# Kernel tuning notes

Measured on AMD Instinct MI355X. Metric: run time of the kernel, lower is better.

## Reference

```python
import jax, jax.numpy as jnp
import numpy as np

POSE_DIM, H_DIM, LATENT_DIM, NUM_LAYERS = 96, 32, 16, 2
BATCH, OBS_LEN, PRED_LEN = 16384, 16, 25


def setup_inputs() -> dict:
    key = jax.random.key(0)
    ks = jax.random.split(key, 16)
    s = 0.1
    inp = {
        "obs_s": jax.random.normal(ks[0], (OBS_LEN, BATCH, POSE_DIM), jnp.float32),
        "latent": jax.random.normal(ks[1], (BATCH, LATENT_DIM), jnp.float32),
        "pred_len": PRED_LEN,
        # FC: latent_dim -> h_dim
        "W_fc": jax.random.normal(ks[2], (H_DIM, LATENT_DIM), jnp.float32) * s,
        "b_fc": jnp.zeros((H_DIM,), jnp.float32),
        # LSTM layer 0 (input pose_dim), PyTorch gate order i,f,g,o
        "W_ih0": jax.random.normal(ks[3], (4 * H_DIM, POSE_DIM), jnp.float32) * s,
        "W_hh0": jax.random.normal(ks[4], (4 * H_DIM, H_DIM), jnp.float32) * s,
        "b_ih0": jax.random.normal(ks[5], (4 * H_DIM,), jnp.float32) * s,
        "b_hh0": jax.random.normal(ks[6], (4 * H_DIM,), jnp.float32) * s,
        # LSTM layer 1 (input h_dim)
        "W_ih1": jax.random.normal(ks[7], (4 * H_DIM, H_DIM), jnp.float32) * s,
        "W_hh1": jax.random.normal(ks[8], (4 * H_DIM, H_DIM), jnp.float32) * s,
        "b_ih1": jax.random.normal(ks[9], (4 * H_DIM,), jnp.float32) * s,
        "b_hh1": jax.random.normal(ks[10], (4 * H_DIM,), jnp.float32) * s,
        # mlp: h_dim -> pose_dim
        "W_mlp": jax.random.normal(ks[11], (POSE_DIM, H_DIM), jnp.float32) * s,
        "b_mlp": jnp.zeros((POSE_DIM,), jnp.float32),
    }
    return inp


def _lstm_cell(x, h, c, W_ih, W_hh, b):
    # x: [B, in], h/c: [B, H]; gates in PyTorch order i, f, g, o
    gates = x @ W_ih.T + h @ W_hh.T + b
    i, f, g, o = jnp.split(gates, 4, axis=-1)
    c_new = jax.nn.sigmoid(f) * c + jax.nn.sigmoid(i) * jnp.tanh(g)
    h_new = jax.nn.sigmoid(o) * jnp.tanh(c_new)
    return h_new, c_new


def reference(obs_s, latent, pred_len, W_fc, b_fc,
              W_ih0, W_hh0, b_ih0, b_hh0,
              W_ih1, W_hh1, b_ih1, b_hh1,
              W_mlp, b_mlp):
    batch = obs_s.shape[1]
    h_init = latent @ W_fc.T + b_fc                    # [B, H] -> both layers
    c0 = jnp.zeros((batch, H_DIM), obs_s.dtype)
    b0 = b_ih0 + b_hh0
    b1 = b_ih1 + b_hh1

    def step(carry, _):
        last, h0, c0_, h1, c1_ = carry
        h0, c0_ = _lstm_cell(last, h0, c0_, W_ih0, W_hh0, b0)
        h1, c1_ = _lstm_cell(h0, h1, c1_, W_ih1, W_hh1, b1)
        curr = h1 @ W_mlp.T + b_mlp                    # [B, pose_dim]
        return (curr, h0, c0_, h1, c1_), curr

    init = (obs_s[-1], h_init, c0, h_init, c0)
    _, preds = jax.lax.scan(step, init, None, length=pred_len)
    return preds  # [pred_len, B, pose_dim]
```

## Files before the change

### kernel.cpp

```cpp
#include <hip/hip_runtime.h>


#define PRED 25
#define BATCH 16384
#define ET    16
#define XROW  192
#define HROW  128
#define LROW  64

typedef unsigned short u16;
typedef unsigned int   u32;
typedef __attribute__((ext_vector_type(8))) short bf16x8;
typedef __attribute__((ext_vector_type(4))) float f32x4;

__device__ __forceinline__ float fast_rcp(float x){ return __builtin_amdgcn_rcpf(x); }
__device__ __forceinline__ float sigm(float x){ return fast_rcp(1.0f + __expf(-x)); }
__device__ __forceinline__ float tanh_(float x){ return 1.0f - 2.0f*fast_rcp(__expf(2.0f*x) + 1.0f); }
__device__ __forceinline__ u16 f2b(float f){
  u32 i = __float_as_uint(f);
  i += 0x7FFFu + ((i >> 16) & 1u);
  return (u16)(i >> 16);
}
__device__ __forceinline__ float b2f(u16 u){ return __uint_as_float(((u32)u) << 16); }

struct __align__(16) SM {
  u16 xh[ET*XROW];
  u16 hh[ET*HROW];
  u16 h1lo[ET*LROW];
};

__device__ __forceinline__ int swx(int e, int k){ return e*XROW + (k ^ ((e&7)<<3)); }
__device__ __forceinline__ int swh(int e, int k){ return e*HROW + (k ^ ((e&7)<<3)); }
__device__ __forceinline__ int swl(int e, int k){ return e*LROW + (k ^ ((e&7)<<3)); }

__device__ __forceinline__ bf16x8 pack8(float4 f0, float4 f1){
  union { bf16x8 v; u16 u8[8]; } fr;
  fr.u8[0]=f2b(f0.x); fr.u8[1]=f2b(f0.y); fr.u8[2]=f2b(f0.z); fr.u8[3]=f2b(f0.w);
  fr.u8[4]=f2b(f1.x); fr.u8[5]=f2b(f1.y); fr.u8[6]=f2b(f1.z); fr.u8[7]=f2b(f1.w);
  return fr.v;
}

extern "C" __global__ __launch_bounds__(128, 2)
void decoder_kernel(const float* __restrict__ obs,  const float* __restrict__ lat,
                    const float* __restrict__ Wfc,  const float* __restrict__ bfc,
                    const float* __restrict__ Wih0, const float* __restrict__ Whh0,
                    const float* __restrict__ bih0, const float* __restrict__ bhh0,
                    const float* __restrict__ Wih1, const float* __restrict__ Whh1,
                    const float* __restrict__ bih1, const float* __restrict__ bhh1,
                    const float* __restrict__ Wmlp, const float* __restrict__ bmlp,
                    float* __restrict__ out)
{
  __shared__ SM sm;
  const int tid = threadIdx.x;
  const int ebase = blockIdx.x * ET;
  const int mh = tid >> 6;
  const int l  = tid & 63;
  const int lr = l & 15;
  const int kq = l >> 4;
  const int e_ln = lr;

  {
    int e = tid >> 3, c8 = (tid & 7)*12;
    const float* src = obs + ((size_t)(15*BATCH) + ebase + e)*96 + c8;
    float4 a = *(const float4*)(src);
    float4 b = *(const float4*)(src+4);
    float4 c = *(const float4*)(src+8);
    float v[12] = {a.x,a.y,a.z,a.w,b.x,b.y,b.z,b.w,c.x,c.y,c.z,c.w};
    #pragma unroll
    for (int j = 0; j < 6; ++j){
      u32 pk = (u32)f2b(v[2*j]) | ((u32)f2b(v[2*j+1]) << 16);
      *(u32*)&sm.xh[swx(e, c8 + 2*j)] = pk;
    }
  }
  {
    int u = tid & 31, eb = (tid >> 5)*4;
    const float* wf = Wfc + u*16;
    float bb = bfc[u];
    #pragma unroll
    for (int e4 = 0; e4 < 4; ++e4){
      int e = eb + e4;
      const float* lp = lat + (size_t)(ebase + e)*16;
      float a = bb;
      #pragma unroll
      for (int j = 0; j < 16; ++j) a = fmaf(wf[j], lp[j], a);
      u16 hb = f2b(a);
      sm.xh[swx(e, 96 + u)] = hb;
      sm.hh[swh(e, 32 + u)] = hb;
    }
  }

  bf16x8 aw0[4][4];
  #pragma unroll
  for (int i = 0; i < 4; ++i){
    int vg = (mh*4 + i)*16 + lr;
    int g  = (vg & 3)*32 + (vg >> 2);
    #pragma unroll
    for (int c = 0; c < 4; ++c){
      int k = c*32 + kq*8;
      const float* src = (k < 96) ? (Wih0 + g*96 + k) : (Whh0 + g*32 + (k - 96));
      aw0[i][c] = pack8(*(const float4*)src, *(const float4*)(src+4));
    }
  }
  bf16x8 aw1[4][2];
  #pragma unroll
  for (int i = 0; i < 4; ++i){
    int vg = (mh*4 + i)*16 + lr;
    int g  = (vg & 3)*32 + (vg >> 2);
    #pragma unroll
    for (int c = 0; c < 2; ++c){
      int k = c*32 + kq*8;
      const float* src = (k < 32) ? (Wih1 + g*32 + k) : (Whh1 + g*32 + (k - 32));
      aw1[i][c] = pack8(*(const float4*)src, *(const float4*)(src+4));
    }
  }
  bf16x8 awm[3];
  #pragma unroll
  for (int i = 0; i < 3; ++i){
    int o = (mh*3 + i)*16 + lr;
    const float* src = Wmlp + o*32 + kq*8;
    awm[i] = pack8(*(const float4*)src, *(const float4*)(src+4));
  }

  f32x4 bias0v[4], bias1v[4];
  #pragma unroll
  for (int i = 0; i < 4; ++i){
    int u = (mh*4 + i)*4 + kq;
    #pragma unroll
    for (int r = 0; r < 4; ++r){
      int g = r*32 + u;
      bias0v[i][r] = bih0[g] + bhh0[g];
      bias1v[i][r] = bih1[g] + bhh1[g];
    }
  }
  f32x4 biasmv[3];
  #pragma unroll
  for (int i = 0; i < 3; ++i){
    int o0 = (mh*3 + i)*16 + kq*4;
    #pragma unroll
    for (int r = 0; r < 4; ++r) biasmv[i][r] = bmlp[o0 + r];
  }

  float c0s[4] = {0.f,0.f,0.f,0.f};
  float c1s[4] = {0.f,0.f,0.f,0.f};

  __syncthreads();

  f32x4 am[3];
  bool have_out = false;
  float* outb = nullptr;

  for (int t = 0; t < PRED; ++t){
    const int p = t & 1;
    bf16x8 bx0 = *(const bf16x8*)&sm.xh[swx(e_ln, 0*32 + kq*8)];
    bf16x8 bx1 = *(const bf16x8*)&sm.xh[swx(e_ln, 1*32 + kq*8)];
    bf16x8 bx2 = *(const bf16x8*)&sm.xh[swx(e_ln, 2*32 + kq*8)];
    bf16x8 bx3 = *(const bf16x8*)&sm.xh[swx(e_ln, 96 + 32*p + kq*8)];
    f32x4 g0[4];
    #pragma unroll
    for (int i = 0; i < 4; ++i){
      f32x4 a = bias0v[i];
      a = __builtin_amdgcn_mfma_f32_16x16x32_bf16(aw0[i][0], bx0, a, 0, 0, 0);
      a = __builtin_amdgcn_mfma_f32_16x16x32_bf16(aw0[i][1], bx1, a, 0, 0, 0);
      a = __builtin_amdgcn_mfma_f32_16x16x32_bf16(aw0[i][2], bx2, a, 0, 0, 0);
      a = __builtin_amdgcn_mfma_f32_16x16x32_bf16(aw0[i][3], bx3, a, 0, 0, 0);
      g0[i] = a;
    }
    #pragma unroll
    for (int i = 0; i < 4; ++i){
      float ig = sigm(g0[i][0]);
      float fg = sigm(g0[i][1]);
      float gg = tanh_(g0[i][2]);
      float og = sigm(g0[i][3]);
      float cn = fmaf(fg, c0s[i], ig*gg);
      c0s[i] = cn;
      u16 hb = f2b(og * tanh_(cn));
      int u = (mh*4 + i)*4 + kq;
      sm.xh[swx(e_ln, 96 + 32*(p^1) + u)] = hb;
      sm.hh[swh(e_ln, u)] = hb;
    }
    __syncthreads();
    bf16x8 bh0 = *(const bf16x8*)&sm.hh[swh(e_ln, kq*8)];
    bf16x8 bh1 = *(const bf16x8*)&sm.hh[swh(e_ln, 32 + 32*p + kq*8)];
    f32x4 g1[4];
    #pragma unroll
    for (int i = 0; i < 4; ++i){
      f32x4 a = bias1v[i];
      a = __builtin_amdgcn_mfma_f32_16x16x32_bf16(aw1[i][0], bh0, a, 0, 0, 0);
      a = __builtin_amdgcn_mfma_f32_16x16x32_bf16(aw1[i][1], bh1, a, 0, 0, 0);
      g1[i] = a;
    }
    #pragma unroll
    for (int i = 0; i < 4; ++i){
      float ig = sigm(g1[i][0]);
      float fg = sigm(g1[i][1]);
      float gg = tanh_(g1[i][2]);
      float og = sigm(g1[i][3]);
      float cn = fmaf(fg, c1s[i], ig*gg);
      c1s[i] = cn;
      float h1 = og * tanh_(cn);
      u16 hi = f2b(h1);
      u16 lo = f2b(h1 - b2f(hi));
      int u = (mh*4 + i)*4 + kq;
      sm.hh[swh(e_ln, 32 + 32*(p^1) + u)] = hi;
      sm.h1lo[swl(e_ln, u)] = lo;
    }
    __syncthreads();
    bf16x8 bmh = *(const bf16x8*)&sm.hh[swh(e_ln, 32 + 32*(p^1) + kq*8)];
    bf16x8 bml = *(const bf16x8*)&sm.h1lo[swl(e_ln, kq*8)];
    #pragma unroll
    for (int i = 0; i < 3; ++i){
      f32x4 a = biasmv[i];
      a = __builtin_amdgcn_mfma_f32_16x16x32_bf16(awm[i], bmh, a, 0, 0, 0);
      a = __builtin_amdgcn_mfma_f32_16x16x32_bf16(awm[i], bml, a, 0, 0, 0);
      am[i] = a;
      int o0 = (mh*3 + i)*16 + kq*4;
      u32 pk01 = (u32)f2b(a[0]) | ((u32)f2b(a[1]) << 16);
      u32 pk23 = (u32)f2b(a[2]) | ((u32)f2b(a[3]) << 16);
      *(u32*)&sm.xh[swx(e_ln, o0)]     = pk01;
      *(u32*)&sm.xh[swx(e_ln, o0 + 2)] = pk23;
    }
    outb = out + (size_t)t*BATCH*96 + (size_t)(ebase + e_ln)*96;
    have_out = true;
    __syncthreads();
    #pragma unroll
    for (int i = 0; i < 3; ++i){
      int o0 = (mh*3 + i)*16 + kq*4;
      *(f32x4*)(outb + o0) = am[i];
    }
  }
  (void)have_out;
}

extern "C" void kernel_launch(void* const* d_in, const int* in_sizes, int n_in,
                              void* d_out, int out_size, void* d_ws, size_t ws_size,
                              hipStream_t stream){
  decoder_kernel<<<dim3(BATCH/ET), dim3(128), 0, stream>>>(
      (const float*)d_in[0],  (const float*)d_in[1],
      (const float*)d_in[3],  (const float*)d_in[4],
      (const float*)d_in[5],  (const float*)d_in[6],
      (const float*)d_in[7],  (const float*)d_in[8],
      (const float*)d_in[9],  (const float*)d_in[10],
      (const float*)d_in[11], (const float*)d_in[12],
      (const float*)d_in[13], (const float*)d_in[14],
      (float*)d_out);
}
```

Measured before the change: 80.56 us.

## Collapse decoder block to a single wave and fold log2e into gate weights

```diff
diff --git a/kernel.cpp b/kernel.cpp
--- a/kernel.cpp
+++ b/kernel.cpp
@@ -3,19 +3,21 @@
 
 #define PRED 25
 #define BATCH 16384
-#define ET    16
-#define XROW  192
-#define HROW  128
-#define LROW  64
+#define SROW 192
 
 typedef unsigned short u16;
 typedef unsigned int   u32;
 typedef __attribute__((ext_vector_type(8))) short bf16x8;
 typedef __attribute__((ext_vector_type(4))) float f32x4;
 
-__device__ __forceinline__ float fast_rcp(float x){ return __builtin_amdgcn_rcpf(x); }
-__device__ __forceinline__ float sigm(float x){ return fast_rcp(1.0f + __expf(-x)); }
-__device__ __forceinline__ float tanh_(float x){ return 1.0f - 2.0f*fast_rcp(__expf(2.0f*x) + 1.0f); }
+#define LOG2E  1.44269504088896340736f
+#define LOG2E2 2.88539008177792681472f
+
+__device__ __forceinline__ float rcp_(float x){ return __builtin_amdgcn_rcpf(x); }
+__device__ __forceinline__ float ex2(float x){ return __builtin_amdgcn_exp2f(x); }
+__device__ __forceinline__ float sigm2(float xp){ return rcp_(1.0f + ex2(-xp)); }
+__device__ __forceinline__ float tanh2(float xp){ return 1.0f - 2.0f*rcp_(ex2(xp) + 1.0f); }
+
 __device__ __forceinline__ u16 f2b(float f){
   u32 i = __float_as_uint(f);
   i += 0x7FFFu + ((i >> 16) & 1u);
@@ -23,24 +25,18 @@
 }
 __device__ __forceinline__ float b2f(u16 u){ return __uint_as_float(((u32)u) << 16); }
 
-struct __align__(16) SM {
-  u16 xh[ET*XROW];
-  u16 hh[ET*HROW];
-  u16 h1lo[ET*LROW];
-};
-
-__device__ __forceinline__ int swx(int e, int k){ return e*XROW + (k ^ ((e&7)<<3)); }
-__device__ __forceinline__ int swh(int e, int k){ return e*HROW + (k ^ ((e&7)<<3)); }
-__device__ __forceinline__ int swl(int e, int k){ return e*LROW + (k ^ ((e&7)<<3)); }
-
-__device__ __forceinline__ bf16x8 pack8(float4 f0, float4 f1){
-  union { bf16x8 v; u16 u8[8]; } fr;
-  fr.u8[0]=f2b(f0.x); fr.u8[1]=f2b(f0.y); fr.u8[2]=f2b(f0.z); fr.u8[3]=f2b(f0.w);
-  fr.u8[4]=f2b(f1.x); fr.u8[5]=f2b(f1.y); fr.u8[6]=f2b(f1.z); fr.u8[7]=f2b(f1.w);
+__device__ __forceinline__ int swz(int e, int k){ return e*SROW + (k ^ ((e&7)<<3)); }
+
+#define LGKM_FENCE() asm volatile("s_waitcnt lgkmcnt(0)" ::: "memory")
+
+__device__ __forceinline__ bf16x8 pack8s(const float* src, float s){
+  union { bf16x8 v; u16 h[8]; } fr;
+  #pragma unroll
+  for (int j = 0; j < 8; ++j) fr.h[j] = f2b(src[j]*s);
   return fr.v;
 }
 
-extern "C" __global__ __launch_bounds__(128, 2)
+extern "C" __global__ __launch_bounds__(64, 1)
 void decoder_kernel(const float* __restrict__ obs,  const float* __restrict__ lat,
                     const float* __restrict__ Wfc,  const float* __restrict__ bfc,
                     const float* __restrict__ Wih0, const float* __restrict__ Whh0,
@@ -50,191 +46,172 @@
                     const float* __restrict__ Wmlp, const float* __restrict__ bmlp,
                     float* __restrict__ out)
 {
-  __shared__ SM sm;
-  const int tid = threadIdx.x;
-  const int ebase = blockIdx.x * ET;
-  const int mh = tid >> 6;
-  const int l  = tid & 63;
+  __shared__ u16 state[16*SROW];
+  const int l  = threadIdx.x;
+  const int ebase = blockIdx.x * 16;
   const int lr = l & 15;
-  const int kq = l >> 4;
-  const int e_ln = lr;
+  const int rq = l >> 4;
 
   {
-    int e = tid >> 3, c8 = (tid & 7)*12;
-    const float* src = obs + ((size_t)(15*BATCH) + ebase + e)*96 + c8;
-    float4 a = *(const float4*)(src);
-    float4 b = *(const float4*)(src+4);
-    float4 c = *(const float4*)(src+8);
-    float v[12] = {a.x,a.y,a.z,a.w,b.x,b.y,b.z,b.w,c.x,c.y,c.z,c.w};
-    #pragma unroll
-    for (int j = 0; j < 6; ++j){
-      u32 pk = (u32)f2b(v[2*j]) | ((u32)f2b(v[2*j+1]) << 16);
-      *(u32*)&sm.xh[swx(e, c8 + 2*j)] = pk;
+    int e = l >> 2, c = (l & 3) * 24;
+    const float* src = obs + ((size_t)(15*BATCH) + ebase + e)*96 + c;
+    #pragma unroll
+    for (int j = 0; j < 12; ++j){
+      float2 v = *(const float2*)(src + 2*j);
+      u32 pk = (u32)f2b(v.x) | ((u32)f2b(v.y) << 16);
+      *(u32*)&state[swz(e, c + 2*j)] = pk;
     }
   }
   {
-    int u = tid & 31, eb = (tid >> 5)*4;
+    int u = l >> 1, eh = (l & 1)*8;
     const float* wf = Wfc + u*16;
     float bb = bfc[u];
     #pragma unroll
-    for (int e4 = 0; e4 < 4; ++e4){
-      int e = eb + e4;
+    for (int r = 0; r < 8; ++r){
+      int e = eh + r;
       const float* lp = lat + (size_t)(ebase + e)*16;
       float a = bb;
       #pragma unroll
       for (int j = 0; j < 16; ++j) a = fmaf(wf[j], lp[j], a);
       u16 hb = f2b(a);
-      sm.xh[swx(e, 96 + u)] = hb;
-      sm.hh[swh(e, 32 + u)] = hb;
-    }
-  }
-
-  bf16x8 aw0[4][4];
-  #pragma unroll
-  for (int i = 0; i < 4; ++i){
-    int vg = (mh*4 + i)*16 + lr;
+      state[swz(e, 96 + u)]  = hb;
+      state[swz(e, 128 + u)] = hb;
+    }
+  }
+
+  bf16x8 aw0[8][4];
+  #pragma unroll
+  for (int i = 0; i < 8; ++i){
+    int vg = i*16 + lr;
     int g  = (vg & 3)*32 + (vg >> 2);
+    float s = ((vg & 3) == 2) ? LOG2E2 : LOG2E;
     #pragma unroll
     for (int c = 0; c < 4; ++c){
-      int k = c*32 + kq*8;
+      int k = c*32 + rq*8;
       const float* src = (k < 96) ? (Wih0 + g*96 + k) : (Whh0 + g*32 + (k - 96));
-      aw0[i][c] = pack8(*(const float4*)src, *(const float4*)(src+4));
-    }
-  }
-  bf16x8 aw1[4][2];
-  #pragma unroll
-  for (int i = 0; i < 4; ++i){
-    int vg = (mh*4 + i)*16 + lr;
+      aw0[i][c] = pack8s(src, s);
+    }
+  }
+  bf16x8 aw1[8][2];
+  #pragma unroll
+  for (int i = 0; i < 8; ++i){
+    int vg = i*16 + lr;
     int g  = (vg & 3)*32 + (vg >> 2);
+    float s = ((vg & 3) == 2) ? LOG2E2 : LOG2E;
     #pragma unroll
     for (int c = 0; c < 2; ++c){
-      int k = c*32 + kq*8;
+      int k = c*32 + rq*8;
       const float* src = (k < 32) ? (Wih1 + g*32 + k) : (Whh1 + g*32 + (k - 32));
-      aw1[i][c] = pack8(*(const float4*)src, *(const float4*)(src+4));
-    }
-  }
-  bf16x8 awm[3];
-  #pragma unroll
-  for (int i = 0; i < 3; ++i){
-    int o = (mh*3 + i)*16 + lr;
-    const float* src = Wmlp + o*32 + kq*8;
-    awm[i] = pack8(*(const float4*)src, *(const float4*)(src+4));
-  }
-
-  f32x4 bias0v[4], bias1v[4];
-  #pragma unroll
-  for (int i = 0; i < 4; ++i){
-    int u = (mh*4 + i)*4 + kq;
+      aw1[i][c] = pack8s(src, s);
+    }
+  }
+  bf16x8 awm[6];
+  #pragma unroll
+  for (int i = 0; i < 6; ++i){
+    int o = i*16 + lr;
+    awm[i] = pack8s(Wmlp + o*32 + rq*8, 1.0f);
+  }
+
+  f32x4 b0v[8], b1v[8];
+  #pragma unroll
+  for (int i = 0; i < 8; ++i){
+    int u = i*4 + rq;
     #pragma unroll
     for (int r = 0; r < 4; ++r){
       int g = r*32 + u;
-      bias0v[i][r] = bih0[g] + bhh0[g];
-      bias1v[i][r] = bih1[g] + bhh1[g];
-    }
-  }
-  f32x4 biasmv[3];
-  #pragma unroll
-  for (int i = 0; i < 3; ++i){
-    int o0 = (mh*3 + i)*16 + kq*4;
-    #pragma unroll
-    for (int r = 0; r < 4; ++r) biasmv[i][r] = bmlp[o0 + r];
-  }
-
-  float c0s[4] = {0.f,0.f,0.f,0.f};
-  float c1s[4] = {0.f,0.f,0.f,0.f};
-
-  __syncthreads();
-
-  f32x4 am[3];
-  bool have_out = false;
-  float* outb = nullptr;
-
+      float s = (r == 2) ? LOG2E2 : LOG2E;
+      b0v[i][r] = (bih0[g] + bhh0[g])*s;
+      b1v[i][r] = (bih1[g] + bhh1[g])*s;
+    }
+  }
+  f32x4 bmv[6];
+  #pragma unroll
+  for (int i = 0; i < 6; ++i){
+    int o0 = i*16 + rq*4;
+    #pragma unroll
+    for (int r = 0; r < 4; ++r) bmv[i][r] = bmlp[o0 + r];
+  }
+
+  float c0s[8] = {0,0,0,0,0,0,0,0};
+  float c1s[8] = {0,0,0,0,0,0,0,0};
+
+  LGKM_FENCE();
+
+  #pragma unroll 1
   for (int t = 0; t < PRED; ++t){
-    const int p = t & 1;
-    bf16x8 bx0 = *(const bf16x8*)&sm.xh[swx(e_ln, 0*32 + kq*8)];
-    bf16x8 bx1 = *(const bf16x8*)&sm.xh[swx(e_ln, 1*32 + kq*8)];
-    bf16x8 bx2 = *(const bf16x8*)&sm.xh[swx(e_ln, 2*32 + kq*8)];
-    bf16x8 bx3 = *(const bf16x8*)&sm.xh[swx(e_ln, 96 + 32*p + kq*8)];
-    f32x4 g0[4];
-    #pragma unroll
-    for (int i = 0; i < 4; ++i){
-      f32x4 a = bias0v[i];
-      a = __builtin_amdgcn_mfma_f32_16x16x32_bf16(aw0[i][0], bx0, a, 0, 0, 0);
-      a = __builtin_amdgcn_mfma_f32_16x16x32_bf16(aw0[i][1], bx1, a, 0, 0, 0);
-      a = __builtin_amdgcn_mfma_f32_16x16x32_bf16(aw0[i][2], bx2, a, 0, 0, 0);
-      a = __builtin_amdgcn_mfma_f32_16x16x32_bf16(aw0[i][3], bx3, a, 0, 0, 0);
+    bf16x8 bx0  = *(const bf16x8*)&state[swz(lr, 0*32 + rq*8)];
+    bf16x8 bx1  = *(const bf16x8*)&state[swz(lr, 1*32 + rq*8)];
+    bf16x8 bx2  = *(const bf16x8*)&state[swz(lr, 2*32 + rq*8)];
+    bf16x8 bh0p = *(const bf16x8*)&state[swz(lr, 96  + rq*8)];
+    bf16x8 bh1p = *(const bf16x8*)&state[swz(lr, 128 + rq*8)];
+    f32x4 g0[8];
+    #pragma unroll
+    for (int i = 0; i < 8; ++i){
+      f32x4 a = b0v[i];
+      a = __builtin_amdgcn_mfma_f32_16x16x32_bf16(aw0[i][0], bx0,  a, 0, 0, 0);
+      a = __builtin_amdgcn_mfma_f32_16x16x32_bf16(aw0[i][1], bx1,  a, 0, 0, 0);
+      a = __builtin_amdgcn_mfma_f32_16x16x32_bf16(aw0[i][2], bx2,  a, 0, 0, 0);
+      a = __builtin_amdgcn_mfma_f32_16x16x32_bf16(aw0[i][3], bh0p, a, 0, 0, 0);
       g0[i] = a;
     }
     #pragma unroll
-    for (int i = 0; i < 4; ++i){
-      float ig = sigm(g0[i][0]);
-      float fg = sigm(g0[i][1]);
-      float gg = tanh_(g0[i][2]);
-      float og = sigm(g0[i][3]);
+    for (int i = 0; i < 8; ++i){
+      float ig = sigm2(g0[i][0]);
+      float fg = sigm2(g0[i][1]);
+      float gg = tanh2(g0[i][2]);
+      float og = sigm2(g0[i][3]);
       float cn = fmaf(fg, c0s[i], ig*gg);
       c0s[i] = cn;
-      u16 hb = f2b(og * tanh_(cn));
-      int u = (mh*4 + i)*4 + kq;
-      sm.xh[swx(e_ln, 96 + 32*(p^1) + u)] = hb;
-      sm.hh[swh(e_ln, u)] = hb;
-    }
-    __syncthreads();
-    bf16x8 bh0 = *(const bf16x8*)&sm.hh[swh(e_ln, kq*8)];
-    bf16x8 bh1 = *(const bf16x8*)&sm.hh[swh(e_ln, 32 + 32*p + kq*8)];
-    f32x4 g1[4];
-    #pragma unroll
-    for (int i = 0; i < 4; ++i){
-      f32x4 a = bias1v[i];
-      a = __builtin_amdgcn_mfma_f32_16x16x32_bf16(aw1[i][0], bh0, a, 0, 0, 0);
-      a = __builtin_amdgcn_mfma_f32_16x16x32_bf16(aw1[i][1], bh1, a, 0, 0, 0);
+      float h = og * tanh2(cn*LOG2E2);
+      state[swz(lr, 96 + i*4 + rq)] = f2b(h);
+    }
+    LGKM_FENCE();
+    bf16x8 bh0n = *(const bf16x8*)&state[swz(lr, 96 + rq*8)];
+    f32x4 g1[8];
+    #pragma unroll
+    for (int i = 0; i < 8; ++i){
+      f32x4 a = b1v[i];
+      a = __builtin_amdgcn_mfma_f32_16x16x32_bf16(aw1[i][0], bh0n, a, 0, 0, 0);
+      a = __builtin_amdgcn_mfma_f32_16x16x32_bf16(aw1[i][1], bh1p, a, 0, 0, 0);
       g1[i] = a;
     }
     #pragma unroll
-    for (int i = 0; i < 4; ++i){
-      float ig = sigm(g1[i][0]);
-      float fg = sigm(g1[i][1]);
-      float gg = tanh_(g1[i][2]);
-      float og = sigm(g1[i][3]);
+    for (int i = 0; i < 8; ++i){
+      float ig = sigm2(g1[i][0]);
+      float fg = sigm2(g1[i][1]);
+      float gg = tanh2(g1[i][2]);
+      float og = sigm2(g1[i][3]);
       float cn = fmaf(fg, c1s[i], ig*gg);
       c1s[i] = cn;
-      float h1 = og * tanh_(cn);
-      u16 hi = f2b(h1);
-      u16 lo = f2b(h1 - b2f(hi));
-      int u = (mh*4 + i)*4 + kq;
-      sm.hh[swh(e_ln, 32 + 32*(p^1) + u)] = hi;
-      sm.h1lo[swl(e_ln, u)] = lo;
-    }
-    __syncthreads();
-    bf16x8 bmh = *(const bf16x8*)&sm.hh[swh(e_ln, 32 + 32*(p^1) + kq*8)];
-    bf16x8 bml = *(const bf16x8*)&sm.h1lo[swl(e_ln, kq*8)];
-    #pragma unroll
-    for (int i = 0; i < 3; ++i){
-      f32x4 a = biasmv[i];
+      float h = og * tanh2(cn*LOG2E2);
+      u16 hi = f2b(h);
+      state[swz(lr, 128 + i*4 + rq)] = hi;
+      state[swz(lr, 160 + i*4 + rq)] = f2b(h - b2f(hi));
+    }
+    LGKM_FENCE();
+    bf16x8 bmh = *(const bf16x8*)&state[swz(lr, 128 + rq*8)];
+    bf16x8 bml = *(const bf16x8*)&state[swz(lr, 160 + rq*8)];
+    float* outb = out + (size_t)t*BATCH*96 + (size_t)(ebase + lr)*96;
+    #pragma unroll
+    for (int i = 0; i < 6; ++i){
+      f32x4 a = bmv[i];
       a = __builtin_amdgcn_mfma_f32_16x16x32_bf16(awm[i], bmh, a, 0, 0, 0);
       a = __builtin_amdgcn_mfma_f32_16x16x32_bf16(awm[i], bml, a, 0, 0, 0);
-      am[i] = a;
-      int o0 = (mh*3 + i)*16 + kq*4;
-      u32 pk01 = (u32)f2b(a[0]) | ((u32)f2b(a[1]) << 16);
-      u32 pk23 = (u32)f2b(a[2]) | ((u32)f2b(a[3]) << 16);
-      *(u32*)&sm.xh[swx(e_ln, o0)]     = pk01;
-      *(u32*)&sm.xh[swx(e_ln, o0 + 2)] = pk23;
-    }
-    outb = out + (size_t)t*BATCH*96 + (size_t)(ebase + e_ln)*96;
-    have_out = true;
-    __syncthreads();
-    #pragma unroll
-    for (int i = 0; i < 3; ++i){
-      int o0 = (mh*3 + i)*16 + kq*4;
-      *(f32x4*)(outb + o0) = am[i];
-    }
-  }
-  (void)have_out;
+      int o0 = i*16 + rq*4;
+      *(f32x4*)(outb + o0) = a;
+      u32 p01 = (u32)f2b(a[0]) | ((u32)f2b(a[1]) << 16);
+      u32 p23 = (u32)f2b(a[2]) | ((u32)f2b(a[3]) << 16);
+      *(u32*)&state[swz(lr, o0)]     = p01;
+      *(u32*)&state[swz(lr, o0 + 2)] = p23;
+    }
+    LGKM_FENCE();
+  }
 }
 
 extern "C" void kernel_launch(void* const* d_in, const int* in_sizes, int n_in,
                               void* d_out, int out_size, void* d_ws, size_t ws_size,
                               hipStream_t stream){
-  decoder_kernel<<<dim3(BATCH/ET), dim3(128), 0, stream>>>(
+  decoder_kernel<<<dim3(BATCH/16), dim3(64), 0, stream>>>(
       (const float*)d_in[0],  (const float*)d_in[1],
       (const float*)d_in[3],  (const float*)d_in[4],
       (const float*)d_in[5],  (const float*)d_in[6],
```

Result: slower. 113.8 us (+41.3%).

## Process two 16-element batch tiles per block and prescale gates for exp2

Applied to the files above, without the earlier changes.

```diff
diff --git a/kernel.cpp b/kernel.cpp
--- a/kernel.cpp
+++ b/kernel.cpp
@@ -3,7 +3,7 @@
 
 #define PRED 25
 #define BATCH 16384
-#define ET    16
+#define ET    32
 #define XROW  192
 #define HROW  128
 #define LROW  64
@@ -13,9 +13,14 @@
 typedef __attribute__((ext_vector_type(8))) short bf16x8;
 typedef __attribute__((ext_vector_type(4))) float f32x4;
 
-__device__ __forceinline__ float fast_rcp(float x){ return __builtin_amdgcn_rcpf(x); }
-__device__ __forceinline__ float sigm(float x){ return fast_rcp(1.0f + __expf(-x)); }
-__device__ __forceinline__ float tanh_(float x){ return 1.0f - 2.0f*fast_rcp(__expf(2.0f*x) + 1.0f); }
+#define LOG2E  1.44269504088896340736f
+#define LOG2E2 2.88539008177792681472f
+
+__device__ __forceinline__ float rcp_(float x){ return __builtin_amdgcn_rcpf(x); }
+__device__ __forceinline__ float ex2(float x){ return __builtin_amdgcn_exp2f(x); }
+__device__ __forceinline__ float sigm2(float xp){ return rcp_(1.0f + ex2(-xp)); }
+__device__ __forceinline__ float tanh2(float xp){ return 1.0f - 2.0f*rcp_(ex2(xp) + 1.0f); }
+
 __device__ __forceinline__ u16 f2b(float f){
   u32 i = __float_as_uint(f);
   i += 0x7FFFu + ((i >> 16) & 1u);
@@ -24,23 +29,23 @@
 __device__ __forceinline__ float b2f(u16 u){ return __uint_as_float(((u32)u) << 16); }
 
 struct __align__(16) SM {
-  u16 xh[ET*XROW];
-  u16 hh[ET*HROW];
-  u16 h1lo[ET*LROW];
+  u16 xh[2][16*XROW];
+  u16 hh[2][16*HROW];
+  u16 h1lo[2][16*LROW];
 };
 
 __device__ __forceinline__ int swx(int e, int k){ return e*XROW + (k ^ ((e&7)<<3)); }
 __device__ __forceinline__ int swh(int e, int k){ return e*HROW + (k ^ ((e&7)<<3)); }
 __device__ __forceinline__ int swl(int e, int k){ return e*LROW + (k ^ ((e&7)<<3)); }
 
-__device__ __forceinline__ bf16x8 pack8(float4 f0, float4 f1){
-  union { bf16x8 v; u16 u8[8]; } fr;
-  fr.u8[0]=f2b(f0.x); fr.u8[1]=f2b(f0.y); fr.u8[2]=f2b(f0.z); fr.u8[3]=f2b(f0.w);
-  fr.u8[4]=f2b(f1.x); fr.u8[5]=f2b(f1.y); fr.u8[6]=f2b(f1.z); fr.u8[7]=f2b(f1.w);
+__device__ __forceinline__ bf16x8 pack8s(const float* src, float s){
+  union { bf16x8 v; u16 h[8]; } fr;
+  #pragma unroll
+  for (int j = 0; j < 8; ++j) fr.h[j] = f2b(src[j]*s);
   return fr.v;
 }
 
-extern "C" __global__ __launch_bounds__(128, 2)
+extern "C" __global__ __launch_bounds__(128, 1)
 void decoder_kernel(const float* __restrict__ obs,  const float* __restrict__ lat,
                     const float* __restrict__ Wfc,  const float* __restrict__ bfc,
                     const float* __restrict__ Wih0, const float* __restrict__ Whh0,
@@ -57,35 +62,32 @@
   const int l  = tid & 63;
   const int lr = l & 15;
   const int kq = l >> 4;
-  const int e_ln = lr;
 
   {
-    int e = tid >> 3, c8 = (tid & 7)*12;
-    const float* src = obs + ((size_t)(15*BATCH) + ebase + e)*96 + c8;
-    float4 a = *(const float4*)(src);
-    float4 b = *(const float4*)(src+4);
-    float4 c = *(const float4*)(src+8);
-    float v[12] = {a.x,a.y,a.z,a.w,b.x,b.y,b.z,b.w,c.x,c.y,c.z,c.w};
-    #pragma unroll
-    for (int j = 0; j < 6; ++j){
-      u32 pk = (u32)f2b(v[2*j]) | ((u32)f2b(v[2*j+1]) << 16);
-      *(u32*)&sm.xh[swx(e, c8 + 2*j)] = pk;
+    int e = tid >> 2, c0 = (tid & 3)*24;
+    int s = e >> 4, er = e & 15;
+    const float* src = obs + ((size_t)(15*BATCH) + ebase + e)*96 + c0;
+    #pragma unroll
+    for (int j = 0; j < 12; ++j){
+      float2 v = *(const float2*)(src + 2*j);
+      u32 pk = (u32)f2b(v.x) | ((u32)f2b(v.y) << 16);
+      *(u32*)&sm.xh[s][swx(er, c0 + 2*j)] = pk;
     }
   }
   {
-    int u = tid & 31, eb = (tid >> 5)*4;
+    int u = tid & 31, e8 = (tid >> 5)*8;
     const float* wf = Wfc + u*16;
     float bb = bfc[u];
     #pragma unroll
-    for (int e4 = 0; e4 < 4; ++e4){
-      int e = eb + e4;
+    for (int r = 0; r < 8; ++r){
+      int e = e8 + r, s = e >> 4, er = e & 15;
       const float* lp = lat + (size_t)(ebase + e)*16;
       float a = bb;
       #pragma unroll
       for (int j = 0; j < 16; ++j) a = fmaf(wf[j], lp[j], a);
       u16 hb = f2b(a);
-      sm.xh[swx(e, 96 + u)] = hb;
-      sm.hh[swh(e, 32 + u)] = hb;
+      sm.xh[s][swx(er, 96 + u)] = hb;
+      sm.hh[s][swh(er, 32 + u)] = hb;
     }
   }
 
@@ -94,11 +96,12 @@
   for (int i = 0; i < 4; ++i){
     int vg = (mh*4 + i)*16 + lr;
     int g  = (vg & 3)*32 + (vg >> 2);
+    float sc = ((vg & 3) == 2) ? LOG2E2 : LOG2E;
     #pragma unroll
     for (int c = 0; c < 4; ++c){
       int k = c*32 + kq*8;
       const float* src = (k < 96) ? (Wih0 + g*96 + k) : (Whh0 + g*32 + (k - 96));
-      aw0[i][c] = pack8(*(const float4*)src, *(const float4*)(src+4));
+      aw0[i][c] = pack8s(src, sc);
     }
   }
   bf16x8 aw1[4][2];
@@ -106,19 +109,19 @@
   for (int i = 0; i < 4; ++i){
     int vg = (mh*4 + i)*16 + lr;
     int g  = (vg & 3)*32 + (vg >> 2);
+    float sc = ((vg & 3) == 2) ? LOG2E2 : LOG2E;
     #pragma unroll
     for (int c = 0; c < 2; ++c){
       int k = c*32 + kq*8;
       const float* src = (k < 32) ? (Wih1 + g*32 + k) : (Whh1 + g*32 + (k - 32));
-      aw1[i][c] = pack8(*(const float4*)src, *(const float4*)(src+4));
+      aw1[i][c] = pack8s(src, sc);
     }
   }
   bf16x8 awm[3];
   #pragma unroll
   for (int i = 0; i < 3; ++i){
     int o = (mh*3 + i)*16 + lr;
-    const float* src = Wmlp + o*32 + kq*8;
-    awm[i] = pack8(*(const float4*)src, *(const float4*)(src+4));
+    awm[i] = pack8s(Wmlp + o*32 + kq*8, 1.0f);
   }
 
   f32x4 bias0v[4], bias1v[4];
@@ -128,8 +131,9 @@
     #pragma unroll
     for (int r = 0; r < 4; ++r){
       int g = r*32 + u;
-      bias0v[i][r] = bih0[g] + bhh0[g];
-      bias1v[i][r] = bih1[g] + bhh1[g];
+      float sc = (r == 2) ? LOG2E2 : LOG2E;
+      bias0v[i][r] = (bih0[g] + bhh0[g])*sc;
+      bias1v[i][r] = (bih1[g] + bhh1[g])*sc;
     }
   }
   f32x4 biasmv[3];
@@ -140,95 +144,107 @@
     for (int r = 0; r < 4; ++r) biasmv[i][r] = bmlp[o0 + r];
   }
 
-  float c0s[4] = {0.f,0.f,0.f,0.f};
-  float c1s[4] = {0.f,0.f,0.f,0.f};
+  float c0s[2][4] = {{0,0,0,0},{0,0,0,0}};
+  float c1s[2][4] = {{0,0,0,0},{0,0,0,0}};
 
   __syncthreads();
 
-  f32x4 am[3];
-  bool have_out = false;
-  float* outb = nullptr;
+  f32x4 am[2][3];
 
   for (int t = 0; t < PRED; ++t){
     const int p = t & 1;
-    bf16x8 bx0 = *(const bf16x8*)&sm.xh[swx(e_ln, 0*32 + kq*8)];
-    bf16x8 bx1 = *(const bf16x8*)&sm.xh[swx(e_ln, 1*32 + kq*8)];
-    bf16x8 bx2 = *(const bf16x8*)&sm.xh[swx(e_ln, 2*32 + kq*8)];
-    bf16x8 bx3 = *(const bf16x8*)&sm.xh[swx(e_ln, 96 + 32*p + kq*8)];
-    f32x4 g0[4];
-    #pragma unroll
-    for (int i = 0; i < 4; ++i){
-      f32x4 a = bias0v[i];
-      a = __builtin_amdgcn_mfma_f32_16x16x32_bf16(aw0[i][0], bx0, a, 0, 0, 0);
-      a = __builtin_amdgcn_mfma_f32_16x16x32_bf16(aw0[i][1], bx1, a, 0, 0, 0);
-      a = __builtin_amdgcn_mfma_f32_16x16x32_bf16(aw0[i][2], bx2, a, 0, 0, 0);
-      a = __builtin_amdgcn_mfma_f32_16x16x32_bf16(aw0[i][3], bx3, a, 0, 0, 0);
-      g0[i] = a;
-    }
-    #pragma unroll
-    for (int i = 0; i < 4; ++i){
-      float ig = sigm(g0[i][0]);
-      float fg = sigm(g0[i][1]);
-      float gg = tanh_(g0[i][2]);
-      float og = sigm(g0[i][3]);
-      float cn = fmaf(fg, c0s[i], ig*gg);
-      c0s[i] = cn;
-      u16 hb = f2b(og * tanh_(cn));
-      int u = (mh*4 + i)*4 + kq;
-      sm.xh[swx(e_ln, 96 + 32*(p^1) + u)] = hb;
-      sm.hh[swh(e_ln, u)] = hb;
-    }
+    f32x4 g0[2][4];
+    #pragma unroll
+    for (int s = 0; s < 2; ++s){
+      bf16x8 bx0 = *(const bf16x8*)&sm.xh[s][swx(lr, 0*32 + kq*8)];
+      bf16x8 bx1 = *(const bf16x8*)&sm.xh[s][swx(lr, 1*32 + kq*8)];
+      bf16x8 bx2 = *(const bf16x8*)&sm.xh[s][swx(lr, 2*32 + kq*8)];
+      bf16x8 bx3 = *(const bf16x8*)&sm.xh[s][swx(lr, 96 + 32*p + kq*8)];
+      #pragma unroll
+      for (int i = 0; i < 4; ++i){
+        f32x4 a = bias0v[i];
+        a = __builtin_amdgcn_mfma_f32_16x16x32_bf16(aw0[i][0], bx0, a, 0, 0, 0);
+        a = __builtin_amdgcn_mfma_f32_16x16x32_bf16(aw0[i][1], bx1, a, 0, 0, 0);
+        a = __builtin_amdgcn_mfma_f32_16x16x32_bf16(aw0[i][2], bx2, a, 0, 0, 0);
+        a = __builtin_amdgcn_mfma_f32_16x16x32_bf16(aw0[i][3], bx3, a, 0, 0, 0);
+        g0[s][i] = a;
+      }
+    }
+    #pragma unroll
+    for (int s = 0; s < 2; ++s)
+      #pragma unroll
+      for (int i = 0; i < 4; ++i){
+        float ig = sigm2(g0[s][i][0]);
+        float fg = sigm2(g0[s][i][1]);
+        float gg = tanh2(g0[s][i][2]);
+        float og = sigm2(g0[s][i][3]);
+        float cn = fmaf(fg, c0s[s][i], ig*gg);
+        c0s[s][i] = cn;
+        u16 hb = f2b(og * tanh2(cn*LOG2E2));
+        int u = (mh*4 + i)*4 + kq;
+        sm.xh[s][swx(lr, 96 + 32*(p^1) + u)] = hb;
+        sm.hh[s][swh(lr, u)] = hb;
+      }
     __syncthreads();
-    bf16x8 bh0 = *(const bf16x8*)&sm.hh[swh(e_ln, kq*8)];
-    bf16x8 bh1 = *(const bf16x8*)&sm.hh[swh(e_ln, 32 + 32*p + kq*8)];
-    f32x4 g1[4];
-    #pragma unroll
-    for (int i = 0; i < 4; ++i){
-      f32x4 a = bias1v[i];
-      a = __builtin_amdgcn_mfma_f32_16x16x32_bf16(aw1[i][0], bh0, a, 0, 0, 0);
-      a = __builtin_amdgcn_mfma_f32_16x16x32_bf16(aw1[i][1], bh1, a, 0, 0, 0);
-      g1[i] = a;
-    }
-    #pragma unroll
-    for (int i = 0; i < 4; ++i){
-      float ig = sigm(g1[i][0]);
-      float fg = sigm(g1[i][1]);
-      float gg = tanh_(g1[i][2]);
-      float og = sigm(g1[i][3]);
-      float cn = fmaf(fg, c1s[i], ig*gg);
-      c1s[i] = cn;
-      float h1 = og * tanh_(cn);
-      u16 hi = f2b(h1);
-      u16 lo = f2b(h1 - b2f(hi));
-      int u = (mh*4 + i)*4 + kq;
-      sm.hh[swh(e_ln, 32 + 32*(p^1) + u)] = hi;
-      sm.h1lo[swl(e_ln, u)] = lo;
-    }
+    f32x4 g1[2][4];
+    #pragma unroll
+    for (int s = 0; s < 2; ++s){
+      bf16x8 bh0 = *(const bf16x8*)&sm.hh[s][swh(lr, kq*8)];
+      bf16x8 bh1 = *(const bf16x8*)&sm.hh[s][swh(lr, 32 + 32*p + kq*8)];
+      #pragma unroll
+      for (int i = 0; i < 4; ++i){
+        f32x4 a = bias1v[i];
+        a = __builtin_amdgcn_mfma_f32_16x16x32_bf16(aw1[i][0], bh0, a, 0, 0, 0);
+        a = __builtin_amdgcn_mfma_f32_16x16x32_bf16(aw1[i][1], bh1, a, 0, 0, 0);
+        g1[s][i] = a;
+      }
+    }
+    #pragma unroll
+    for (int s = 0; s < 2; ++s)
+      #pragma unroll
+      for (int i = 0; i < 4; ++i){
+        float ig = sigm2(g1[s][i][0]);
+        float fg = sigm2(g1[s][i][1]);
+        float gg = tanh2(g1[s][i][2]);
+        float og = sigm2(g1[s][i][3]);
+        float cn = fmaf(fg, c1s[s][i], ig*gg);
+        c1s[s][i] = cn;
+        float h1 = og * tanh2(cn*LOG2E2);
+        u16 hi = f2b(h1);
+        u16 lo = f2b(h1 - b2f(hi));
+        int u = (mh*4 + i)*4 + kq;
+        sm.hh[s][swh(lr, 32 + 32*(p^1) + u)] = hi;
+        sm.h1lo[s][swl(lr, u)] = lo;
+      }
     __syncthreads();
-    bf16x8 bmh = *(const bf16x8*)&sm.hh[swh(e_ln, 32 + 32*(p^1) + kq*8)];
-    bf16x8 bml = *(const bf16x8*)&sm.h1lo[swl(e_ln, kq*8)];
-    #pragma unroll
-    for (int i = 0; i < 3; ++i){
-      f32x4 a = biasmv[i];
-      a = __builtin_amdgcn_mfma_f32_16x16x32_bf16(awm[i], bmh, a, 0, 0, 0);
-      a = __builtin_amdgcn_mfma_f32_16x16x32_bf16(awm[i], bml, a, 0, 0, 0);
-      am[i] = a;
-      int o0 = (mh*3 + i)*16 + kq*4;
-      u32 pk01 = (u32)f2b(a[0]) | ((u32)f2b(a[1]) << 16);
-      u32 pk23 = (u32)f2b(a[2]) | ((u32)f2b(a[3]) << 16);
-      *(u32*)&sm.xh[swx(e_ln, o0)]     = pk01;
-      *(u32*)&sm.xh[swx(e_ln, o0 + 2)] = pk23;
-    }
-    outb = out + (size_t)t*BATCH*96 + (size_t)(ebase + e_ln)*96;
-    have_out = true;
+    #pragma unroll
+    for (int s = 0; s < 2; ++s){
+      bf16x8 bmh = *(const bf16x8*)&sm.hh[s][swh(lr, 32 + 32*(p^1) + kq*8)];
+      bf16x8 bml = *(const bf16x8*)&sm.h1lo[s][swl(lr, kq*8)];
+      #pragma unroll
+      for (int i = 0; i < 3; ++i){
+        f32x4 a = biasmv[i];
+        a = __builtin_amdgcn_mfma_f32_16x16x32_bf16(awm[i], bmh, a, 0, 0, 0);
+        a = __builtin_amdgcn_mfma_f32_16x16x32_bf16(awm[i], bml, a, 0, 0, 0);
+        am[s][i] = a;
+        int o0 = (mh*3 + i)*16 + kq*4;
+        u32 pk01 = (u32)f2b(a[0]) | ((u32)f2b(a[1]) << 16);
+        u32 pk23 = (u32)f2b(a[2]) | ((u32)f2b(a[3]) << 16);
+        *(u32*)&sm.xh[s][swx(lr, o0)]     = pk01;
+        *(u32*)&sm.xh[s][swx(lr, o0 + 2)] = pk23;
+      }
+    }
     __syncthreads();
     #pragma unroll
-    for (int i = 0; i < 3; ++i){
-      int o0 = (mh*3 + i)*16 + kq*4;
-      *(f32x4*)(outb + o0) = am[i];
-    }
-  }
-  (void)have_out;
+    for (int s = 0; s < 2; ++s){
+      float* outb = out + (size_t)t*BATCH*96 + (size_t)(ebase + s*16 + lr)*96;
+      #pragma unroll
+      for (int i = 0; i < 3; ++i){
+        int o0 = (mh*3 + i)*16 + kq*4;
+        *(f32x4*)(outb + o0) = am[s][i];
+      }
+    }
+  }
 }
 
 extern "C" void kernel_launch(void* const* d_in, const int* in_sizes, int n_in,
```

Result: faster. 78.76 us (-2.2%).
